# Kernel optimization log

Hardware: AMD Instinct MI355X
Metric: run time of the kernel (lower is better)

## Reference

```python
import jax, jax.numpy as jnp
import numpy as np
from jax import lax

ITER, L, D, H = 8, 4096, 512, 256


def setup_inputs() -> dict:
    key = jax.random.key(0)
    ks = jax.random.split(key, 12)
    sD = 1.0 / np.sqrt(D)
    sH = 1.0 / np.sqrt(H)
    return {
        "embeddings_seq": jax.random.normal(ks[0], (ITER, L, D), jnp.float32),
        "ROIs": jax.random.uniform(ks[1], (1, L, 3), jnp.float32),
        "Wx": jax.random.normal(ks[2], (L, D), jnp.float32) * sD,
        "bx": jax.random.normal(ks[3], (L,), jnp.float32) * 0.01,
        "Wy": jax.random.normal(ks[4], (L, D), jnp.float32) * sD,
        "by": jax.random.normal(ks[5], (L,), jnp.float32) * 0.01,
        "Wz": jax.random.normal(ks[6], (L, D), jnp.float32) * sD,
        "bz": jax.random.normal(ks[7], (L,), jnp.float32) * 0.01,
        "Ws": jax.random.normal(ks[8], (D, H), jnp.float32) * sD,
        "bs": jax.random.normal(ks[9], (H,), jnp.float32) * 0.01,
        "Wh": jax.random.normal(ks[10], (L, H), jnp.float32) * sH,
        "bh": jax.random.normal(ks[11], (L,), jnp.float32) * 0.01,
    }


def reference(embeddings_seq, ROIs, Wx, bx, Wy, by, Wz, bz, Ws, bs, Wh, bh):
    # size_tensor = [1/767, 1/767, 1/575]
    size = jnp.array([1.0 / 767, 1.0 / 767, 1.0 / 575], dtype=embeddings_seq.dtype)

    def dec(h):  # grouped Conv1d(k=D, groups=L) == per-landmark dot product; h: [L, D]
        x = jnp.sum(Wx * h, axis=-1) + bx
        y = jnp.sum(Wy * h, axis=-1) + by
        z = jnp.sum(Wz * h, axis=-1) + bz
        return jnp.stack([x, y, z], axis=-1)  # [L, 3]

    def gate_head(h):  # Linear+Tanh shared, then per-landmark grouped conv; h: [L, D]
        s = jnp.tanh(h @ Ws + bs)          # [L, H]
        return jnp.sum(Wh * s, axis=-1) + bh  # [L]

    emb0 = embeddings_seq[0]                  # [L, D]
    rois0 = ROIs[0]                           # [L, 3]
    predict0 = dec(emb0) * size + rois0       # [L, 3]

    def step(carry, emb):
        h, c, pred = carry
        rois = pred                           # previous prediction becomes new ROIs
        gf = gate_head(h)                     # [L]
        ga = gate_head(emb)                   # [L]
        g = jax.nn.softmax(jnp.stack([gf, ga], axis=-1), axis=-1)  # [L, 2]
        g0, g1 = g[:, 0:1], g[:, 1:2]
        h = h * g0 + emb * g1
        c = c * g0 + rois * g1
        pred = dec(h) * size + lax.stop_gradient(c)
        return (h, c, pred), pred

    init = (emb0, rois0, predict0)
    _, preds = lax.scan(step, init, embeddings_seq[1:])  # [ITER-1, L, 3]
    return jnp.concatenate([predict0[None], preds], axis=0)  # [ITER, L, 3]
```

## Files before the change

kernel.cpp:

```cpp
#include <hip/hip_runtime.h>
#include <stdint.h>

#define L_DIM 4096
#define D_DIM 512
#define H_DIM 256
#define T_DIM 8

typedef short bf16x8 __attribute__((ext_vector_type(8)));
typedef float f32x4 __attribute__((ext_vector_type(4)));

__device__ __forceinline__ unsigned short f2bf(float f) {
    union { float f; unsigned int u; } c; c.f = f;
    unsigned int u = c.u;
    unsigned int r = (u + 0x7fffu + ((u >> 16) & 1u)) >> 16;
    return (unsigned short)r;
}

__device__ __forceinline__ float bits2f(unsigned int u) {
    union { unsigned int u; float f; } c; c.u = u; return c.f;
}

__device__ __forceinline__ float4 unpack_bf4(uint2 q) {
    float4 r;
    r.x = bits2f(q.x << 16);
    r.y = bits2f(q.x & 0xffff0000u);
    r.z = bits2f(q.y << 16);
    r.w = bits2f(q.y & 0xffff0000u);
    return r;
}

__device__ __forceinline__ float wave_sum(float x) {
    #pragma unroll
    for (int off = 32; off > 0; off >>= 1) x += __shfl_xor(x, off, 64);
    return x;
}

__device__ __forceinline__ float dot4(float4 a, float4 b) {
    return a.x * b.x + a.y * b.y + a.z * b.z + a.w * b.w;
}

__device__ __forceinline__ float fast_tanh(float x) {
    float e = __expf(2.0f * x);
    return 1.0f - 2.0f / (e + 1.0f);
}

__device__ __forceinline__ float4 tanh4b(float4 a, float4 b) {
    float4 r;
    r.x = fast_tanh(a.x + b.x); r.y = fast_tanh(a.y + b.y);
    r.z = fast_tanh(a.z + b.z); r.w = fast_tanh(a.w + b.w);
    return r;
}

__global__ void k_transpose_ws(const float* __restrict__ Ws,
                               unsigned short* __restrict__ WsT) {
    int idx = blockIdx.x * 256 + threadIdx.x;
    int j = idx >> 9;
    int k = idx & 511;
    WsT[idx] = f2bf(Ws[k * H_DIM + j]);
}

__global__ __launch_bounds__(512, 4) void k_gemm_v(
    const float* __restrict__ emb,
    const unsigned short* __restrict__ WsT,
    unsigned short* __restrict__ v) {
    __shared__ __align__(16) char smem[81920];

    const int tid  = threadIdx.x;
    const int lane = tid & 63;
    const int wid  = tid >> 6;
    const int wm   = wid >> 2;
    const int wn   = wid & 3;
    const long rowBase = (long)blockIdx.x * 64;

    const int arow = tid >> 4, aq = tid & 15;
    const int bj   = tid >> 3, bko = tid & 7;
    const float*          ag = emb + (rowBase + arow) * D_DIM + aq * 4;
    const unsigned short* bg = WsT + (long)bj * D_DIM + bko * 8;

    const int adst0 = arow * 128 + ((aq * 8) ^ ((arow & 7) << 4));
    const int adst1 = (arow + 32) * 128 + ((aq * 8) ^ (((arow + 32) & 7) << 4));
    const int bdst[4] = {
        bj * 128 + ((bko * 16) ^ ((bj & 7) << 4)),
        (bj + 64) * 128 + ((bko * 16) ^ (((bj + 64) & 7) << 4)),
        (bj + 128) * 128 + ((bko * 16) ^ (((bj + 128) & 7) << 4)),
        (bj + 192) * 128 + ((bko * 16) ^ (((bj + 192) & 7) << 4))};

    f32x4 acc[2][4];
    #pragma unroll
    for (int mi = 0; mi < 2; mi++)
        #pragma unroll
        for (int ni = 0; ni < 4; ni++) acc[mi][ni] = (f32x4){0.f, 0.f, 0.f, 0.f};

    {
        float4 a0 = *(const float4*)(ag);
        float4 a1 = *(const float4*)(ag + 32 * D_DIM);
        char* As = smem;
        char* Bs = smem + 8192;
        uint2 p0, p1;
        p0.x = (unsigned)f2bf(a0.x) | ((unsigned)f2bf(a0.y) << 16);
        p0.y = (unsigned)f2bf(a0.z) | ((unsigned)f2bf(a0.w) << 16);
        p1.x = (unsigned)f2bf(a1.x) | ((unsigned)f2bf(a1.y) << 16);
        p1.y = (unsigned)f2bf(a1.z) | ((unsigned)f2bf(a1.w) << 16);
        *(uint2*)(As + adst0) = p0;
        *(uint2*)(As + adst1) = p1;
        #pragma unroll
        for (int p = 0; p < 4; p++)
            *(uint4*)(Bs + bdst[p]) = *(const uint4*)(bg + (long)p * 64 * D_DIM);
    }
    __syncthreads();

    #pragma unroll
    for (int kt = 0; kt < 8; ++kt) {
        char* As = smem + (kt & 1) * 40960;
        char* Bs = As + 8192;
        char* Asn = smem + ((kt + 1) & 1) * 40960;
        char* Bsn = Asn + 8192;

        float4 a0, a1;
        uint4 b0, b1, b2, b3;
        if (kt < 7) {
            const float* ap = ag + (kt + 1) * 64;
            a0 = *(const float4*)(ap);
            a1 = *(const float4*)(ap + 32 * D_DIM);
            const unsigned short* bp = bg + (kt + 1) * 64;
            b0 = *(const uint4*)(bp);
            b1 = *(const uint4*)(bp + (long)64 * D_DIM);
            b2 = *(const uint4*)(bp + (long)128 * D_DIM);
            b3 = *(const uint4*)(bp + (long)192 * D_DIM);
        }

        #pragma unroll
        for (int ks = 0; ks < 2; ++ks) {
            bf16x8 a[2], b[4];
            #pragma unroll
            for (int mi = 0; mi < 2; mi++) {
                int row = wm * 32 + mi * 16 + (lane & 15);
                a[mi] = *(const bf16x8*)(As + row * 128 +
                          (((ks * 64) + (lane >> 4) * 16) ^ ((row & 7) << 4)));
            }
            #pragma unroll
            for (int ni = 0; ni < 4; ni++) {
                int j = wn * 64 + ni * 16 + (lane & 15);
                b[ni] = *(const bf16x8*)(Bs + j * 128 +
                          (((ks * 64) + (lane >> 4) * 16) ^ ((j & 7) << 4)));
            }
            #pragma unroll
            for (int mi = 0; mi < 2; mi++)
                #pragma unroll
                for (int ni = 0; ni < 4; ni++)
                    acc[mi][ni] = __builtin_amdgcn_mfma_f32_16x16x32_bf16(
                        a[mi], b[ni], acc[mi][ni], 0, 0, 0);
        }

        if (kt < 7) {
            uint2 p0, p1;
            p0.x = (unsigned)f2bf(a0.x) | ((unsigned)f2bf(a0.y) << 16);
            p0.y = (unsigned)f2bf(a0.z) | ((unsigned)f2bf(a0.w) << 16);
            p1.x = (unsigned)f2bf(a1.x) | ((unsigned)f2bf(a1.y) << 16);
            p1.y = (unsigned)f2bf(a1.z) | ((unsigned)f2bf(a1.w) << 16);
            *(uint2*)(Asn + adst0) = p0;
            *(uint2*)(Asn + adst1) = p1;
            *(uint4*)(Bsn + bdst[0]) = b0;
            *(uint4*)(Bsn + bdst[1]) = b1;
            *(uint4*)(Bsn + bdst[2]) = b2;
            *(uint4*)(Bsn + bdst[3]) = b3;
        }
        __syncthreads();
    }

    #pragma unroll
    for (int mi = 0; mi < 2; mi++)
        #pragma unroll
        for (int ni = 0; ni < 4; ni++)
            #pragma unroll
            for (int r = 0; r < 4; r++) {
                long row = rowBase + wm * 32 + mi * 16 + (lane >> 4) * 4 + r;
                int  col = wn * 64 + ni * 16 + (lane & 15);
                v[row * H_DIM + col] = f2bf(acc[mi][ni][r]);
            }
}

__global__ __launch_bounds__(256) void k_seq(
    const float* __restrict__ emb, const float* __restrict__ rois,
    const float* __restrict__ Wx, const float* __restrict__ bx,
    const float* __restrict__ Wy, const float* __restrict__ by,
    const float* __restrict__ Wz, const float* __restrict__ bz,
    const float* __restrict__ bs, const float* __restrict__ Wh,
    const float* __restrict__ bh, const unsigned short* __restrict__ v,
    float* __restrict__ out) {
    const int lane = threadIdx.x & 63;
    const int l = blockIdx.x * 4 + (threadIdx.x >> 6);
    const int j4 = lane * 4;
    const int d8 = lane * 8;

    float4 Wh4 = *(const float4*)(Wh + (long)l * H_DIM + j4);
    float4 bs4 = *(const float4*)(bs + j4);
    float4 wx0 = *(const float4*)(Wx + (long)l * D_DIM + d8);
    float4 wx1 = *(const float4*)(Wx + (long)l * D_DIM + d8 + 4);
    float4 wy0 = *(const float4*)(Wy + (long)l * D_DIM + d8);
    float4 wy1 = *(const float4*)(Wy + (long)l * D_DIM + d8 + 4);
    float4 wz0 = *(const float4*)(Wz + (long)l * D_DIM + d8);
    float4 wz1 = *(const float4*)(Wz + (long)l * D_DIM + d8 + 4);
    float bxl = bx[l], byl = by[l], bzl = bz[l], bhl = bh[l];
    const float sx = 1.f / 767.f, sy = 1.f / 767.f, sz = 1.f / 575.f;

    float px[T_DIM], py[T_DIM], pz[T_DIM], ga[T_DIM];
    uint2 vvp[T_DIM];
    #pragma unroll
    for (int t = 0; t < T_DIM; ++t) {
        const float* eb = emb + ((long)t * L_DIM + l) * D_DIM + d8;
        float4 f0 = *(const float4*)(eb);
        float4 f1 = *(const float4*)(eb + 4);
        px[t] = dot4(wx0, f0) + dot4(wx1, f1);
        py[t] = dot4(wy0, f0) + dot4(wy1, f1);
        pz[t] = dot4(wz0, f0) + dot4(wz1, f1);
        uint2 q = *(const uint2*)(v + ((long)t * L_DIM + l) * H_DIM + j4);
        vvp[t] = q;
        float4 sa = tanh4b(unpack_bf4(q), bs4);
        ga[t] = dot4(Wh4, sa);
    }
    #pragma unroll
    for (int t = 0; t < T_DIM; ++t) {
        px[t] = wave_sum(px[t]);
        py[t] = wave_sum(py[t]);
        pz[t] = wave_sum(pz[t]);
        ga[t] = wave_sum(ga[t]) + bhl;
    }

    float4 u4 = unpack_bf4(vvp[0]);
    float cx = rois[l * 3 + 0], cy = rois[l * 3 + 1], cz = rois[l * 3 + 2];
    float dx = px[0], dy = py[0], dz = pz[0];
    float prx = (dx + bxl) * sx + cx;
    float pry = (dy + byl) * sy + cy;
    float prz = (dz + bzl) * sz + cz;
    if (lane == 0) {
        out[l * 3 + 0] = prx; out[l * 3 + 1] = pry; out[l * 3 + 2] = prz;
    }

    #pragma unroll
    for (int t = 1; t < T_DIM; ++t) {
        float4 sf = tanh4b(u4, bs4);
        float gf = wave_sum(dot4(Wh4, sf)) + bhl;

        float g0 = 1.0f / (1.0f + __expf(ga[t] - gf));
        float g1 = 1.0f - g0;

        float4 v4 = unpack_bf4(vvp[t]);
        u4.x = g0 * u4.x + g1 * v4.x; u4.y = g0 * u4.y + g1 * v4.y;
        u4.z = g0 * u4.z + g1 * v4.z; u4.w = g0 * u4.w + g1 * v4.w;

        cx = cx * g0 + prx * g1; cy = cy * g0 + pry * g1; cz = cz * g0 + prz * g1;
        dx = g0 * dx + g1 * px[t]; dy = g0 * dy + g1 * py[t]; dz = g0 * dz + g1 * pz[t];

        prx = (dx + bxl) * sx + cx;
        pry = (dy + byl) * sy + cy;
        prz = (dz + bzl) * sz + cz;
        if (lane == 0) {
            float* o = out + (long)t * (L_DIM * 3) + l * 3;
            o[0] = prx; o[1] = pry; o[2] = prz;
        }
    }
}

extern "C" void kernel_launch(void* const* d_in, const int* in_sizes, int n_in,
                              void* d_out, int out_size, void* d_ws, size_t ws_size,
                              hipStream_t stream) {
    const float* emb  = (const float*)d_in[0];
    const float* rois = (const float*)d_in[1];
    const float* Wx   = (const float*)d_in[2];
    const float* bx   = (const float*)d_in[3];
    const float* Wy   = (const float*)d_in[4];
    const float* by   = (const float*)d_in[5];
    const float* Wz   = (const float*)d_in[6];
    const float* bz   = (const float*)d_in[7];
    const float* Ws   = (const float*)d_in[8];
    const float* bs   = (const float*)d_in[9];
    const float* Wh   = (const float*)d_in[10];
    const float* bh   = (const float*)d_in[11];
    float* out = (float*)d_out;

    unsigned short* v   = (unsigned short*)d_ws;
    unsigned short* WsT = (unsigned short*)((char*)d_ws + (size_t)16 * 1024 * 1024);

    hipLaunchKernelGGL(k_transpose_ws, dim3(512), dim3(256), 0, stream, Ws, WsT);
    hipLaunchKernelGGL(k_gemm_v, dim3(512), dim3(512), 0, stream, emb, WsT, v);
    hipLaunchKernelGGL(k_seq, dim3(1024), dim3(256), 0, stream,
                       emb, rois, Wx, bx, Wy, by, Wz, bz, bs, Wh, bh, v, out);
}
```

Baseline: 167.0 us.

## Fuse gate GEMM and sequential recurrence into one kernel via LDS

Merges the bf16 MFMA GEMM that computes emb@Ws with the per-landmark recurrence kernel. Each block now handles 8 landmarks across all 8 timesteps, so the 64-row GEMM tile is regrouped by landmark and the result stays in shared memory instead of a global workspace. This removes the 16 MB bf16 intermediate write and read-back and one kernel launch. In exchange each block does more serial work, only 512 blocks run the recurrence phase, and the second phase is limited by the GEMM kernel's occupancy and LDS footprint.

```diff
diff --git a/kernel.cpp b/kernel.cpp
--- a/kernel.cpp
+++ b/kernel.cpp
@@ -59,10 +59,14 @@
     WsT[idx] = f2bf(Ws[k * H_DIM + j]);
 }
 
-__global__ __launch_bounds__(512, 4) void k_gemm_v(
-    const float* __restrict__ emb,
-    const unsigned short* __restrict__ WsT,
-    unsigned short* __restrict__ v) {
+__global__ __launch_bounds__(512, 4) void k_fused(
+    const float* __restrict__ emb, const float* __restrict__ rois,
+    const float* __restrict__ Wx, const float* __restrict__ bx,
+    const float* __restrict__ Wy, const float* __restrict__ by,
+    const float* __restrict__ Wz, const float* __restrict__ bz,
+    const float* __restrict__ bs, const float* __restrict__ Wh,
+    const float* __restrict__ bh, const unsigned short* __restrict__ WsT,
+    float* __restrict__ out) {
     __shared__ __align__(16) char smem[81920];
 
     const int tid  = threadIdx.x;
@@ -70,15 +74,16 @@
     const int wid  = tid >> 6;
     const int wm   = wid >> 2;
     const int wn   = wid & 3;
-    const long rowBase = (long)blockIdx.x * 64;
+    const int lbase = blockIdx.x * 8;
 
     const int arow = tid >> 4, aq = tid & 15;
-    const int bj   = tid >> 3, bko = tid & 7;
-    const float*          ag = emb + (rowBase + arow) * D_DIM + aq * 4;
-    const unsigned short* bg = WsT + (long)bj * D_DIM + bko * 8;
-
+    const int t0 = arow >> 3, li0 = arow & 7;
+    const float* ag0 = emb + ((long)t0 * L_DIM + lbase + li0) * D_DIM + aq * 4;
+    const float* ag1 = ag0 + (long)4 * L_DIM * D_DIM;
     const int adst0 = arow * 128 + ((aq * 8) ^ ((arow & 7) << 4));
     const int adst1 = (arow + 32) * 128 + ((aq * 8) ^ (((arow + 32) & 7) << 4));
+    const int bj = tid >> 3, bko = tid & 7;
+    const unsigned short* bg = WsT + (long)bj * D_DIM + bko * 8;
     const int bdst[4] = {
         bj * 128 + ((bko * 16) ^ ((bj & 7) << 4)),
         (bj + 64) * 128 + ((bko * 16) ^ (((bj + 64) & 7) << 4)),
@@ -92,8 +97,8 @@
         for (int ni = 0; ni < 4; ni++) acc[mi][ni] = (f32x4){0.f, 0.f, 0.f, 0.f};
 
     {
-        float4 a0 = *(const float4*)(ag);
-        float4 a1 = *(const float4*)(ag + 32 * D_DIM);
+        float4 a0 = *(const float4*)(ag0);
+        float4 a1 = *(const float4*)(ag1);
         char* As = smem;
         char* Bs = smem + 8192;
         uint2 p0, p1;
@@ -119,9 +124,10 @@
         float4 a0, a1;
         uint4 b0, b1, b2, b3;
         if (kt < 7) {
-            const float* ap = ag + (kt + 1) * 64;
-            a0 = *(const float4*)(ap);
-            a1 = *(const float4*)(ap + 32 * D_DIM);
+            const float* ap0 = ag0 + (kt + 1) * 64;
+            const float* ap1 = ag1 + (kt + 1) * 64;
+            a0 = *(const float4*)(ap0);
+            a1 = *(const float4*)(ap1);
             const unsigned short* bp = bg + (kt + 1) * 64;
             b0 = *(const uint4*)(bp);
             b1 = *(const uint4*)(bp + (long)64 * D_DIM);
@@ -168,28 +174,20 @@
         __syncthreads();
     }
 
+    unsigned short* v_lds = (unsigned short*)smem;
     #pragma unroll
     for (int mi = 0; mi < 2; mi++)
         #pragma unroll
         for (int ni = 0; ni < 4; ni++)
             #pragma unroll
             for (int r = 0; r < 4; r++) {
-                long row = rowBase + wm * 32 + mi * 16 + (lane >> 4) * 4 + r;
-                int  col = wn * 64 + ni * 16 + (lane & 15);
-                v[row * H_DIM + col] = f2bf(acc[mi][ni][r]);
+                int row = wm * 32 + mi * 16 + (lane >> 4) * 4 + r;
+                int col = wn * 64 + ni * 16 + (lane & 15);
+                v_lds[row * H_DIM + col] = f2bf(acc[mi][ni][r]);
             }
-}
-
-__global__ __launch_bounds__(256) void k_seq(
-    const float* __restrict__ emb, const float* __restrict__ rois,
-    const float* __restrict__ Wx, const float* __restrict__ bx,
-    const float* __restrict__ Wy, const float* __restrict__ by,
-    const float* __restrict__ Wz, const float* __restrict__ bz,
-    const float* __restrict__ bs, const float* __restrict__ Wh,
-    const float* __restrict__ bh, const unsigned short* __restrict__ v,
-    float* __restrict__ out) {
-    const int lane = threadIdx.x & 63;
-    const int l = blockIdx.x * 4 + (threadIdx.x >> 6);
+    __syncthreads();
+
+    const int l = lbase + wid;
     const int j4 = lane * 4;
     const int d8 = lane * 8;
 
@@ -204,8 +202,12 @@
     float bxl = bx[l], byl = by[l], bzl = bz[l], bhl = bh[l];
     const float sx = 1.f / 767.f, sy = 1.f / 767.f, sz = 1.f / 575.f;
 
+    uint2 vvp[T_DIM];
+    #pragma unroll
+    for (int t = 0; t < T_DIM; ++t)
+        vvp[t] = *(const uint2*)(v_lds + (t * 8 + wid) * H_DIM + j4);
+
     float px[T_DIM], py[T_DIM], pz[T_DIM], ga[T_DIM];
-    uint2 vvp[T_DIM];
     #pragma unroll
     for (int t = 0; t < T_DIM; ++t) {
         const float* eb = emb + ((long)t * L_DIM + l) * D_DIM + d8;
@@ -214,9 +216,7 @@
         px[t] = dot4(wx0, f0) + dot4(wx1, f1);
         py[t] = dot4(wy0, f0) + dot4(wy1, f1);
         pz[t] = dot4(wz0, f0) + dot4(wz1, f1);
-        uint2 q = *(const uint2*)(v + ((long)t * L_DIM + l) * H_DIM + j4);
-        vvp[t] = q;
-        float4 sa = tanh4b(unpack_bf4(q), bs4);
+        float4 sa = tanh4b(unpack_bf4(vvp[t]), bs4);
         ga[t] = dot4(Wh4, sa);
     }
     #pragma unroll
@@ -279,11 +279,9 @@
     const float* bh   = (const float*)d_in[11];
     float* out = (float*)d_out;
 
-    unsigned short* v   = (unsigned short*)d_ws;
-    unsigned short* WsT = (unsigned short*)((char*)d_ws + (size_t)16 * 1024 * 1024);
+    unsigned short* WsT = (unsigned short*)d_ws;
 
     hipLaunchKernelGGL(k_transpose_ws, dim3(512), dim3(256), 0, stream, Ws, WsT);
-    hipLaunchKernelGGL(k_gemm_v, dim3(512), dim3(512), 0, stream, emb, WsT, v);
-    hipLaunchKernelGGL(k_seq, dim3(1024), dim3(256), 0, stream,
-                       emb, rois, Wx, bx, Wy, by, Wz, bz, bs, Wh, bh, v, out);
-}
+    hipLaunchKernelGGL(k_fused, dim3(512), dim3(512), 0, stream,
+                       emb, rois, Wx, bx, Wy, by, Wz, bz, bs, Wh, bh, WsT, out);
+}
```

Measured after the change: 153.8 us. -7.9%, faster.
